# Kernel optimization log

Measured on AMD Instinct MI355X. Metric: run time of the kernel, lower is better.

Reference implementation:

```python
import jax, jax.numpy as jnp
import numpy as np

NEG = -9e15  # fill value used by the torch module for invalid band locations


def _sliding_window_attention(q, k, v, w, padding_mask):
    """Banded (Longformer-style) attention.
    q, k, v: [B, H, S, d]; padding_mask: [B, S] (nonzero = valid).
    S must be a multiple of 2*w (matches the no-extra-padding path of the
    original module). Returns context [B, H, S, d].
    """
    B, H, S, d = q.shape
    nb = S // w  # number of query blocks of size w
    # Query blocks: [B, H, nb, w, d]
    q_c = q.reshape(B, H, nb, w, d)
    # Each query block attends to a 3w-wide key/value slab (w halo each side).
    idx = (jnp.arange(nb) * w)[:, None] + jnp.arange(3 * w)[None, :]  # [nb, 3w]
    k_pad = jnp.pad(k, ((0, 0), (0, 0), (w, w), (0, 0)))
    v_pad = jnp.pad(v, ((0, 0), (0, 0), (w, w), (0, 0)))
    k_c = k_pad[:, :, idx, :]  # [B, H, nb, 3w, d]
    v_c = v_pad[:, :, idx, :]  # [B, H, nb, 3w, d]
    # Block scores: [B, H, nb, w, 3w]
    scores3 = jnp.einsum('bhnxd,bhnyd->bhnxy', q_c, k_c)
    # Extract the (2w+1)-wide band: query local x, band offset j -> slab col x+j
    x_idx = jnp.arange(w)[:, None]                     # [w, 1]
    j_idx = x_idx + jnp.arange(2 * w + 1)[None, :]     # [w, 2w+1], values in [0, 3w-1]
    band = scores3[..., x_idx, j_idx]                  # [B, H, nb, w, 2w+1]
    # Validity: global key position i - w + j must lie in [0, S) and be unpadded.
    key_pos = jnp.arange(S).reshape(nb, w)[:, :, None] - w + jnp.arange(2 * w + 1)
    valid = (key_pos >= 0) & (key_pos < S)                       # [nb, w, 2w+1]
    kmask = padding_mask[:, jnp.clip(key_pos, 0, S - 1)] != 0    # [B, nb, w, 2w+1]
    m = valid[None, None] & kmask[:, None]                       # [B, H, nb, w, 2w+1]
    band = jnp.where(m, band, NEG)
    # Original scales by sqrt(q.shape[-1]) == sqrt(head_dim)
    attn = jax.nn.softmax(band / jnp.sqrt(jnp.asarray(d, band.dtype)), axis=-1)
    attn = jnp.where(m, attn, 0.0)  # mirrors the explicit softmax_mask zeroing
    # Scatter band back to slab layout and contract with values.
    attn3 = jnp.zeros_like(scores3).at[..., x_idx, j_idx].set(attn)
    ctx = jnp.einsum('bhnxy,bhnyd->bhnxd', attn3, v_c)
    return ctx.reshape(B, H, S, d)


def setup_inputs() -> dict:
    key = jax.random.key(0)
    k0, k1, k2 = jax.random.split(key, 3)
    B, S, D, E = 2, 4096, 1024, 1024
    x = jax.random.normal(k0, (B, S, D), jnp.float32)
    padding_mask = jnp.ones((B, S), jnp.int32)
    # xavier_uniform like the torch _reset_parameters; biases zero
    s_qkv = (6.0 / (D + 3 * E)) ** 0.5
    Wqkv = jax.random.uniform(k1, (3 * E, D), jnp.float32, -s_qkv, s_qkv)
    bqkv = jnp.zeros((3 * E,), jnp.float32)
    s_o = (6.0 / (E + E)) ** 0.5
    Wo = jax.random.uniform(k2, (E, E), jnp.float32, -s_o, s_o)
    bo = jnp.zeros((E,), jnp.float32)
    return {'x': x, 'padding_mask': padding_mask, 'Wqkv': Wqkv, 'bqkv': bqkv,
            'Wo': Wo, 'bo': bo}


def reference(x, padding_mask, Wqkv, bqkv, Wo, bo):
    B, S, D = x.shape
    E = Wo.shape[0]
    H = 16
    hd = E // H
    w = 512 // 2  # window_size // 2
    qkv = (x @ Wqkv.T + bqkv).reshape(B, S, H, 3, hd)
    q = jnp.transpose(qkv[..., 0, :], (0, 2, 1, 3))  # [B, H, S, hd]
    k = jnp.transpose(qkv[..., 1, :], (0, 2, 1, 3))
    v = jnp.transpose(qkv[..., 2, :], (0, 2, 1, 3))
    ctx = _sliding_window_attention(q, k, v, w, padding_mask)
    out = jnp.transpose(ctx, (0, 2, 1, 3)).reshape(B, S, E)
    return out @ Wo.T + bo
```

## Files before the change

### kernel.cpp

```cpp
#include <hip/hip_runtime.h>
#include <stdint.h>

typedef __attribute__((ext_vector_type(8))) short short8;
typedef __attribute__((ext_vector_type(4))) float f32x4;

__device__ __forceinline__ unsigned short f2bf(float f) {
  unsigned int u = __builtin_bit_cast(unsigned int, f);
  u += 0x7FFFu + ((u >> 16) & 1u);
  return (unsigned short)(u >> 16);
}

#define GLD_LDS16(gp, lp) \
  __builtin_amdgcn_global_load_lds((const __attribute__((address_space(1))) void*)(gp), \
                                   (__attribute__((address_space(3))) void*)(lp), 16, 0, 0)

__global__ __launch_bounds__(256) void cvt_all_kernel(
    const float* __restrict__ x, const float* __restrict__ Wqkv, const float* __restrict__ Wo,
    unsigned short* __restrict__ xb, unsigned short* __restrict__ Wqkvb,
    unsigned short* __restrict__ Wob) {
  int i = blockIdx.x * 256 + threadIdx.x;
  const float* src; unsigned short* dst; int local; float scale = 1.0f;
  if (i < 1048576) { src = x; dst = xb; local = i; }
  else if (i < 1048576 + 393216) {
    local = i - 1048576; src = Wqkv; dst = Wqkvb;
    int row = (local * 8) >> 10;
    if (((row >> 6) % 3) == 0) scale = 0.125f;
  } else { local = i - 1441792; src = Wo; dst = Wob; }
  const float4* s4 = (const float4*)src;
  float4 a = s4[local * 2], b = s4[local * 2 + 1];
  uint4 o;
  o.x = (unsigned)f2bf(a.x * scale) | ((unsigned)f2bf(a.y * scale) << 16);
  o.y = (unsigned)f2bf(a.z * scale) | ((unsigned)f2bf(a.w * scale) << 16);
  o.z = (unsigned)f2bf(b.x * scale) | ((unsigned)f2bf(b.y * scale) << 16);
  o.w = (unsigned)f2bf(b.z * scale) | ((unsigned)f2bf(b.w * scale) << 16);
  *(uint4*)(dst + (size_t)local * 8) = o;
}

template<int EPI>
__global__ __launch_bounds__(256, 2) void gemm_bt(
    const unsigned short* __restrict__ A, const unsigned short* __restrict__ Bw,
    const float* __restrict__ bias, void* o0, void* o1, void* o2,
    int M, int N, int K, int nbc)
{
  __shared__ __align__(16) unsigned short Asm[128 * 64];
  __shared__ __align__(16) unsigned short Bsm[128 * 64];
  int bid = blockIdx.x;
  int bc = bid % nbc, br = bid / nbc;
  int tid = threadIdx.x;
  int lane = tid & 63, w = tid >> 6;
  int l16 = lane & 15, g = lane >> 4;
  int wr = w >> 1, wc = w & 1;
  f32x4 acc[4][4];
  #pragma unroll
  for (int i = 0; i < 4; i++)
    #pragma unroll
    for (int j = 0; j < 4; j++) acc[i][j] = (f32x4){0.f, 0.f, 0.f, 0.f};

  const int nkt = K >> 6;
  for (int kt = 0; kt < nkt; ++kt) {
    __syncthreads();
    #pragma unroll
    for (int r = 0; r < 4; ++r) {
      int idx = tid + 256 * r;
      int row = idx >> 3, s = idx & 7;
      int gofs = ((s ^ (row & 7)) << 3) + (kt << 6);
      GLD_LDS16(A + (size_t)(br * 128 + row) * K + gofs, &Asm[idx << 3]);
      GLD_LDS16(Bw + (size_t)(bc * 128 + row) * K + gofs, &Bsm[idx << 3]);
    }
    __syncthreads();
    #pragma unroll
    for (int kk = 0; kk < 2; ++kk) {
      short8 af[4], bf[4];
      #pragma unroll
      for (int i = 0; i < 4; i++) {
        int rowa = wr * 64 + i * 16 + l16;
        af[i] = *(const short8*)&Asm[(rowa << 6) + ((((kk << 2) + g) ^ (rowa & 7)) << 3)];
        int rowb = wc * 64 + i * 16 + l16;
        bf[i] = *(const short8*)&Bsm[(rowb << 6) + ((((kk << 2) + g) ^ (rowb & 7)) << 3)];
      }
      #pragma unroll
      for (int i = 0; i < 4; i++)
        #pragma unroll
        for (int j = 0; j < 4; j++)
          acc[i][j] = __builtin_amdgcn_mfma_f32_16x16x32_bf16(af[i], bf[j], acc[i][j], 0, 0, 0);
    }
  }
  #pragma unroll
  for (int i = 0; i < 4; i++) {
    #pragma unroll
    for (int j = 0; j < 4; j++) {
      int n = bc * 128 + wc * 64 + j * 16 + l16;
      int m0 = br * 128 + wr * 64 + i * 16 + g * 4;
      if (EPI == 0) {
        int t = (n >> 6) % 3;
        int hh = n / 192, e = n & 63;
        float bval = bias[n]; if (t == 0) bval *= 0.125f;
        int bb = m0 >> 12, s0 = m0 & 4095;
        if (t == 2) {
          unsigned short p0 = f2bf(acc[i][j][0] + bval);
          unsigned short p1 = f2bf(acc[i][j][1] + bval);
          unsigned short p2 = f2bf(acc[i][j][2] + bval);
          unsigned short p3 = f2bf(acc[i][j][3] + bval);
          uint2 pk;
          pk.x = (unsigned)p0 | ((unsigned)p1 << 16);
          pk.y = (unsigned)p2 | ((unsigned)p3 << 16);
          unsigned short* vt = (unsigned short*)o2;
          *(uint2*)&vt[(((size_t)(bb * 16 + hh) * 64 + e) << 12) + s0] = pk;
        } else {
          unsigned short* dst = (unsigned short*)(t == 0 ? o0 : o1);
          #pragma unroll
          for (int jj = 0; jj < 4; jj++)
            dst[((((size_t)(bb * 16 + hh) << 12) + s0 + jj) << 6) + e] = f2bf(acc[i][j][jj] + bval);
        }
      } else {
        float* o = (float*)o0;
        float bval = bias[n];
        #pragma unroll
        for (int jj = 0; jj < 4; jj++)
          o[(size_t)(m0 + jj) * N + n] = acc[i][j][jj] + bval;
      }
    }
  }
}

__global__ __launch_bounds__(256, 4) void attn_kernel(
    const unsigned short* __restrict__ qb, const unsigned short* __restrict__ kb,
    const unsigned short* __restrict__ vtb, const int* __restrict__ pmask,
    unsigned short* __restrict__ ctxb)
{
  const int S = 4096, HD = 64, WIN = 256;
  const float NEG = -1e38f;
  __shared__ __align__(16) unsigned short Ks[2][64 * 64];
  __shared__ __align__(16) unsigned short Vts[2][64 * 64];
  __shared__ __align__(16) unsigned short Ps[4][16 * 64];

  int bid0 = blockIdx.x;
  int bid = (bid0 & 7) * (gridDim.x >> 3) + (bid0 >> 3);
  int qt = bid & 63;
  int bh = bid >> 6;
  int b = bh >> 4, h = bh & 15;

  const unsigned short* Q  = qb + (size_t)bh * S * HD;
  const unsigned short* Kg = kb + (size_t)bh * S * HD;
  const unsigned short* Vt = vtb + (size_t)bh * HD * S;
  const int* pmrow = pmask + (size_t)b * S;

  int tid = threadIdx.x;
  int lane = tid & 63, w = tid >> 6;
  int l16 = lane & 15, g = lane >> 4;

  int q0 = qt * 64;
  int qw = q0 + w * 16;

  short8 qf[2];
  #pragma unroll
  for (int hh = 0; hh < 2; ++hh)
    qf[hh] = *(const short8*)&Q[(size_t)(qw + l16) * HD + hh * 32 + g * 8];

  f32x4 ctx[4];
  #pragma unroll
  for (int dt = 0; dt < 4; ++dt) ctx[dt] = (f32x4){0.f, 0.f, 0.f, 0.f};
  float lrun[4] = {0.f, 0.f, 0.f, 0.f};

  int kt0 = (q0 - WIN) >> 6; if (kt0 < 0) kt0 = 0;
  int kt1 = (q0 + 63 + WIN) >> 6; if (kt1 > 63) kt1 = 63;
  int nt = kt1 - kt0 + 1;

#define STAGE(BUF, KT) do {                                                       \
    int kb_ = (KT) * 64;                                                          \
    _Pragma("unroll")                                                             \
    for (int r_ = 0; r_ < 2; ++r_) {                                              \
      int idx_ = tid + 256 * r_;                                                  \
      int row_ = idx_ >> 3, s_ = idx_ & 7;                                        \
      int c_ = (s_ ^ (row_ & 7)) << 3;                                            \
      GLD_LDS16(Kg + (size_t)(kb_ + row_) * HD + c_, &Ks[BUF][idx_ << 3]);        \
      GLD_LDS16(Vt + (size_t)row_ * S + kb_ + c_, &Vts[BUF][idx_ << 3]);          \
    }                                                                             \
  } while (0)

  STAGE(0, kt0);
  asm volatile("s_waitcnt vmcnt(0)" ::: "memory");
  __syncthreads();

  int cur = 0;
  for (int it = 0; it < nt; ++it) {
    int kbase = (kt0 + it) * 64;
    if (it + 1 < nt) STAGE(cur ^ 1, kt0 + it + 1);

    float kbv[4];
    #pragma unroll
    for (int k4 = 0; k4 < 4; ++k4)
      kbv[k4] = (pmrow[kbase + k4 * 16 + l16] != 0) ? 0.f : NEG;

    f32x4 sc[4];
    __builtin_amdgcn_s_setprio(1);
    #pragma unroll
    for (int k4 = 0; k4 < 4; ++k4) {
      int krow = k4 * 16 + l16;
      f32x4 s = (f32x4){0.f, 0.f, 0.f, 0.f};
      short8 kf0 = *(const short8*)&Ks[cur][(krow << 6) + ((g ^ (l16 & 7)) << 3)];
      s = __builtin_amdgcn_mfma_f32_16x16x32_bf16(qf[0], kf0, s, 0, 0, 0);
      short8 kf1 = *(const short8*)&Ks[cur][(krow << 6) + (((4 + g) ^ (l16 & 7)) << 3)];
      s = __builtin_amdgcn_mfma_f32_16x16x32_bf16(qf[1], kf1, s, 0, 0, 0);
      sc[k4] = s;
    }
    __builtin_amdgcn_s_setprio(0);

    #pragma unroll
    for (int k4 = 0; k4 < 4; ++k4) {
      int kg = kbase + k4 * 16 + l16;
      #pragma unroll
      for (int jj = 0; jj < 4; ++jj) {
        int dq = kg - (qw + g * 4 + jj) + WIN;
        float sv = sc[k4][jj] + kbv[k4];
        sv = ((unsigned)dq <= 2u * WIN) ? sv : NEG;
        float p = __expf(sv);
        lrun[jj] += p;
        int row = g * 4 + jj, col = k4 * 16 + l16;
        Ps[w][(row << 6) + ((((col >> 3) ^ (row & 7)) << 3) | (col & 7))] = f2bf(p);
      }
    }

    asm volatile("s_waitcnt lgkmcnt(0)" ::: "memory");
    __builtin_amdgcn_sched_barrier(0);
    short8 pf0 = *(const short8*)&Ps[w][(l16 << 6) + ((g ^ (l16 & 7)) << 3)];
    short8 pf1 = *(const short8*)&Ps[w][(l16 << 6) + (((4 + g) ^ (l16 & 7)) << 3)];
    __builtin_amdgcn_s_setprio(1);
    #pragma unroll
    for (int dt = 0; dt < 4; ++dt) {
      int drow = dt * 16 + l16;
      short8 vf0 = *(const short8*)&Vts[cur][(drow << 6) + ((g ^ (drow & 7)) << 3)];
      ctx[dt] = __builtin_amdgcn_mfma_f32_16x16x32_bf16(pf0, vf0, ctx[dt], 0, 0, 0);
      short8 vf1 = *(const short8*)&Vts[cur][(drow << 6) + (((4 + g) ^ (drow & 7)) << 3)];
      ctx[dt] = __builtin_amdgcn_mfma_f32_16x16x32_bf16(pf1, vf1, ctx[dt], 0, 0, 0);
    }
    __builtin_amdgcn_s_setprio(0);

    if (it + 1 < nt) {
      asm volatile("s_waitcnt vmcnt(0)" ::: "memory");
      __syncthreads();
      cur ^= 1;
    }
  }
#undef STAGE

  #pragma unroll
  for (int jj = 0; jj < 4; ++jj) {
    float ps = lrun[jj];
    #pragma unroll
    for (int mk = 1; mk < 16; mk <<= 1) ps += __shfl_xor(ps, mk);
    lrun[jj] = ps;
  }

  #pragma unroll
  for (int jj = 0; jj < 4; ++jj) {
    float rc = (lrun[jj] > 0.f) ? (1.f / lrun[jj]) : 0.f;
    int qrow = qw + g * 4 + jj;
    size_t base = ((size_t)b * S + qrow) * 1024 + h * 64;
    #pragma unroll
    for (int dt = 0; dt < 4; ++dt)
      ctxb[base + dt * 16 + l16] = f2bf(ctx[dt][jj] * rc);
  }
}

extern "C" void kernel_launch(void* const* d_in, const int* in_sizes, int n_in,
                              void* d_out, int out_size, void* d_ws, size_t ws_size,
                              hipStream_t stream) {
  const float* x     = (const float*)d_in[0];
  const int*   pmask = (const int*)d_in[1];
  const float* Wqkv  = (const float*)d_in[2];
  const float* bqkv  = (const float*)d_in[3];
  const float* Wo    = (const float*)d_in[4];
  const float* bo    = (const float*)d_in[5];

  char* wsp = (char*)d_ws;
  unsigned short* xb    = (unsigned short*)(wsp);
  unsigned short* Wqkvb = (unsigned short*)(wsp + (size_t)(16u << 20));
  unsigned short* Wob   = (unsigned short*)(wsp + (size_t)(22u << 20));
  unsigned short* vtb   = (unsigned short*)(wsp + (size_t)(24u << 20));
  unsigned short* ctxb  = (unsigned short*)(wsp + (size_t)(40u << 20));
  unsigned short* qbuf  = (unsigned short*)d_out;
  unsigned short* kbuf  = (unsigned short*)d_out + (size_t)8388608;

  cvt_all_kernel<<<6144, 256, 0, stream>>>(x, Wqkv, Wo, xb, Wqkvb, Wob);

  gemm_bt<0><<<(8192 / 128) * (3072 / 128), 256, 0, stream>>>(
      xb, Wqkvb, bqkv, qbuf, kbuf, vtb, 8192, 3072, 1024, 3072 / 128);

  attn_kernel<<<2048, 256, 0, stream>>>(qbuf, kbuf, vtb, pmask, ctxb);

  gemm_bt<1><<<(8192 / 128) * (1024 / 128), 256, 0, stream>>>(
      ctxb, Wob, bo, d_out, nullptr, nullptr, 8192, 1024, 1024, 1024 / 128);
}
```

Before: 146.7 us.

## Enlarge attention query tile to 256 rows with 8 waves sharing K/V tiles

Each attention block now covers 256 queries with 512 threads (8 waves, 32 query rows each as two 16-row subtiles) instead of 64 queries with 4 waves. K/V tiles are staged once per block and reused across more queries, so the halo of redundant key/value loads per block shrinks from 9 tiles per 64 queries to 12 tiles per 256 queries. The cost is larger blocks, more registers per wave (double accumulators), a grid of only 512 blocks, and the 256-query tile overlapping more fully-masked key tiles at the band edges, which can waste MFMA work.

```diff
diff --git a/kernel.cpp b/kernel.cpp
--- a/kernel.cpp
+++ b/kernel.cpp
@@ -123,7 +123,7 @@
   }
 }
 
-__global__ __launch_bounds__(256, 4) void attn_kernel(
+__global__ __launch_bounds__(512, 6) void attn_kernel(
     const unsigned short* __restrict__ qb, const unsigned short* __restrict__ kb,
     const unsigned short* __restrict__ vtb, const int* __restrict__ pmask,
     unsigned short* __restrict__ ctxb)
@@ -132,12 +132,12 @@
   const float NEG = -1e38f;
   __shared__ __align__(16) unsigned short Ks[2][64 * 64];
   __shared__ __align__(16) unsigned short Vts[2][64 * 64];
-  __shared__ __align__(16) unsigned short Ps[4][16 * 64];
+  __shared__ __align__(16) unsigned short Ps[8][16 * 64];
 
   int bid0 = blockIdx.x;
   int bid = (bid0 & 7) * (gridDim.x >> 3) + (bid0 >> 3);
-  int qt = bid & 63;
-  int bh = bid >> 6;
+  int qt = bid & 15;
+  int bh = bid >> 4;
   int b = bh >> 4, h = bh & 15;
 
   const unsigned short* Q  = qb + (size_t)bh * S * HD;
@@ -149,33 +149,33 @@
   int lane = tid & 63, w = tid >> 6;
   int l16 = lane & 15, g = lane >> 4;
 
-  int q0 = qt * 64;
-  int qw = q0 + w * 16;
-
-  short8 qf[2];
-  #pragma unroll
-  for (int hh = 0; hh < 2; ++hh)
-    qf[hh] = *(const short8*)&Q[(size_t)(qw + l16) * HD + hh * 32 + g * 8];
-
-  f32x4 ctx[4];
-  #pragma unroll
-  for (int dt = 0; dt < 4; ++dt) ctx[dt] = (f32x4){0.f, 0.f, 0.f, 0.f};
-  float lrun[4] = {0.f, 0.f, 0.f, 0.f};
+  int q0 = qt * 256;
+  int qw = q0 + w * 32;
+
+  short8 qf[2][2];
+  #pragma unroll
+  for (int qs = 0; qs < 2; ++qs)
+    #pragma unroll
+    for (int hh = 0; hh < 2; ++hh)
+      qf[qs][hh] = *(const short8*)&Q[(size_t)(qw + qs * 16 + l16) * HD + hh * 32 + g * 8];
+
+  f32x4 ctx[2][4];
+  #pragma unroll
+  for (int qs = 0; qs < 2; ++qs)
+    #pragma unroll
+    for (int dt = 0; dt < 4; ++dt) ctx[qs][dt] = (f32x4){0.f, 0.f, 0.f, 0.f};
+  float lrun[2][4] = {{0.f,0.f,0.f,0.f},{0.f,0.f,0.f,0.f}};
 
   int kt0 = (q0 - WIN) >> 6; if (kt0 < 0) kt0 = 0;
-  int kt1 = (q0 + 63 + WIN) >> 6; if (kt1 > 63) kt1 = 63;
+  int kt1 = (q0 + 255 + WIN) >> 6; if (kt1 > 63) kt1 = 63;
   int nt = kt1 - kt0 + 1;
 
 #define STAGE(BUF, KT) do {                                                       \
     int kb_ = (KT) * 64;                                                          \
-    _Pragma("unroll")                                                             \
-    for (int r_ = 0; r_ < 2; ++r_) {                                              \
-      int idx_ = tid + 256 * r_;                                                  \
-      int row_ = idx_ >> 3, s_ = idx_ & 7;                                        \
-      int c_ = (s_ ^ (row_ & 7)) << 3;                                            \
-      GLD_LDS16(Kg + (size_t)(kb_ + row_) * HD + c_, &Ks[BUF][idx_ << 3]);        \
-      GLD_LDS16(Vt + (size_t)row_ * S + kb_ + c_, &Vts[BUF][idx_ << 3]);          \
-    }                                                                             \
+    int row_ = tid >> 3, s_ = tid & 7;                                            \
+    int c_ = (s_ ^ (row_ & 7)) << 3;                                              \
+    GLD_LDS16(Kg + (size_t)(kb_ + row_) * HD + c_, &Ks[BUF][tid << 3]);           \
+    GLD_LDS16(Vt + (size_t)row_ * S + kb_ + c_, &Vts[BUF][tid << 3]);             \
   } while (0)
 
   STAGE(0, kt0);
@@ -192,49 +192,53 @@
     for (int k4 = 0; k4 < 4; ++k4)
       kbv[k4] = (pmrow[kbase + k4 * 16 + l16] != 0) ? 0.f : NEG;
 
-    f32x4 sc[4];
-    __builtin_amdgcn_s_setprio(1);
-    #pragma unroll
-    for (int k4 = 0; k4 < 4; ++k4) {
-      int krow = k4 * 16 + l16;
-      f32x4 s = (f32x4){0.f, 0.f, 0.f, 0.f};
-      short8 kf0 = *(const short8*)&Ks[cur][(krow << 6) + ((g ^ (l16 & 7)) << 3)];
-      s = __builtin_amdgcn_mfma_f32_16x16x32_bf16(qf[0], kf0, s, 0, 0, 0);
-      short8 kf1 = *(const short8*)&Ks[cur][(krow << 6) + (((4 + g) ^ (l16 & 7)) << 3)];
-      s = __builtin_amdgcn_mfma_f32_16x16x32_bf16(qf[1], kf1, s, 0, 0, 0);
-      sc[k4] = s;
-    }
-    __builtin_amdgcn_s_setprio(0);
-
-    #pragma unroll
-    for (int k4 = 0; k4 < 4; ++k4) {
-      int kg = kbase + k4 * 16 + l16;
-      #pragma unroll
-      for (int jj = 0; jj < 4; ++jj) {
-        int dq = kg - (qw + g * 4 + jj) + WIN;
-        float sv = sc[k4][jj] + kbv[k4];
-        sv = ((unsigned)dq <= 2u * WIN) ? sv : NEG;
-        float p = __expf(sv);
-        lrun[jj] += p;
-        int row = g * 4 + jj, col = k4 * 16 + l16;
-        Ps[w][(row << 6) + ((((col >> 3) ^ (row & 7)) << 3) | (col & 7))] = f2bf(p);
-      }
-    }
-
-    asm volatile("s_waitcnt lgkmcnt(0)" ::: "memory");
-    __builtin_amdgcn_sched_barrier(0);
-    short8 pf0 = *(const short8*)&Ps[w][(l16 << 6) + ((g ^ (l16 & 7)) << 3)];
-    short8 pf1 = *(const short8*)&Ps[w][(l16 << 6) + (((4 + g) ^ (l16 & 7)) << 3)];
-    __builtin_amdgcn_s_setprio(1);
-    #pragma unroll
-    for (int dt = 0; dt < 4; ++dt) {
-      int drow = dt * 16 + l16;
-      short8 vf0 = *(const short8*)&Vts[cur][(drow << 6) + ((g ^ (drow & 7)) << 3)];
-      ctx[dt] = __builtin_amdgcn_mfma_f32_16x16x32_bf16(pf0, vf0, ctx[dt], 0, 0, 0);
-      short8 vf1 = *(const short8*)&Vts[cur][(drow << 6) + (((4 + g) ^ (drow & 7)) << 3)];
-      ctx[dt] = __builtin_amdgcn_mfma_f32_16x16x32_bf16(pf1, vf1, ctx[dt], 0, 0, 0);
-    }
-    __builtin_amdgcn_s_setprio(0);
+    #pragma unroll
+    for (int qs = 0; qs < 2; ++qs) {
+      f32x4 sc[4];
+      __builtin_amdgcn_s_setprio(1);
+      #pragma unroll
+      for (int k4 = 0; k4 < 4; ++k4) {
+        int krow = k4 * 16 + l16;
+        f32x4 s = (f32x4){0.f, 0.f, 0.f, 0.f};
+        short8 kf0 = *(const short8*)&Ks[cur][(krow << 6) + ((g ^ (l16 & 7)) << 3)];
+        s = __builtin_amdgcn_mfma_f32_16x16x32_bf16(qf[qs][0], kf0, s, 0, 0, 0);
+        short8 kf1 = *(const short8*)&Ks[cur][(krow << 6) + (((4 + g) ^ (l16 & 7)) << 3)];
+        s = __builtin_amdgcn_mfma_f32_16x16x32_bf16(qf[qs][1], kf1, s, 0, 0, 0);
+        sc[k4] = s;
+      }
+      __builtin_amdgcn_s_setprio(0);
+
+      int qbase = qw + qs * 16 + g * 4;
+      #pragma unroll
+      for (int k4 = 0; k4 < 4; ++k4) {
+        int kg = kbase + k4 * 16 + l16;
+        #pragma unroll
+        for (int jj = 0; jj < 4; ++jj) {
+          int dq = kg - (qbase + jj) + WIN;
+          float sv = sc[k4][jj] + kbv[k4];
+          sv = ((unsigned)dq <= 2u * WIN) ? sv : NEG;
+          float p = __expf(sv);
+          lrun[qs][jj] += p;
+          int row = g * 4 + jj, col = k4 * 16 + l16;
+          Ps[w][(row << 6) + ((((col >> 3) ^ (row & 7)) << 3) | (col & 7))] = f2bf(p);
+        }
+      }
+
+      asm volatile("s_waitcnt lgkmcnt(0)" ::: "memory");
+      __builtin_amdgcn_sched_barrier(0);
+      short8 pf0 = *(const short8*)&Ps[w][(l16 << 6) + ((g ^ (l16 & 7)) << 3)];
+      short8 pf1 = *(const short8*)&Ps[w][(l16 << 6) + (((4 + g) ^ (l16 & 7)) << 3)];
+      __builtin_amdgcn_s_setprio(1);
+      #pragma unroll
+      for (int dt = 0; dt < 4; ++dt) {
+        int drow = dt * 16 + l16;
+        short8 vf0 = *(const short8*)&Vts[cur][(drow << 6) + ((g ^ (drow & 7)) << 3)];
+        ctx[qs][dt] = __builtin_amdgcn_mfma_f32_16x16x32_bf16(pf0, vf0, ctx[qs][dt], 0, 0, 0);
+        short8 vf1 = *(const short8*)&Vts[cur][(drow << 6) + (((4 + g) ^ (drow & 7)) << 3)];
+        ctx[qs][dt] = __builtin_amdgcn_mfma_f32_16x16x32_bf16(pf1, vf1, ctx[qs][dt], 0, 0, 0);
+      }
+      __builtin_amdgcn_s_setprio(0);
+    }
 
     if (it + 1 < nt) {
       asm volatile("s_waitcnt vmcnt(0)" ::: "memory");
@@ -245,21 +249,19 @@
 #undef STAGE
 
   #pragma unroll
-  for (int jj = 0; jj < 4; ++jj) {
-    float ps = lrun[jj];
-    #pragma unroll
-    for (int mk = 1; mk < 16; mk <<= 1) ps += __shfl_xor(ps, mk);
-    lrun[jj] = ps;
-  }
-
-  #pragma unroll
-  for (int jj = 0; jj < 4; ++jj) {
-    float rc = (lrun[jj] > 0.f) ? (1.f / lrun[jj]) : 0.f;
-    int qrow = qw + g * 4 + jj;
-    size_t base = ((size_t)b * S + qrow) * 1024 + h * 64;
-    #pragma unroll
-    for (int dt = 0; dt < 4; ++dt)
-      ctxb[base + dt * 16 + l16] = f2bf(ctx[dt][jj] * rc);
+  for (int qs = 0; qs < 2; ++qs) {
+    #pragma unroll
+    for (int jj = 0; jj < 4; ++jj) {
+      float ps = lrun[qs][jj];
+      #pragma unroll
+      for (int mk = 1; mk < 16; mk <<= 1) ps += __shfl_xor(ps, mk);
+      float rc = (ps > 0.f) ? (1.f / ps) : 0.f;
+      int qrow = qw + qs * 16 + g * 4 + jj;
+      size_t base = ((size_t)b * S + qrow) * 1024 + h * 64;
+      #pragma unroll
+      for (int dt = 0; dt < 4; ++dt)
+        ctxb[base + dt * 16 + l16] = f2bf(ctx[qs][dt][jj] * rc);
+    }
   }
 }
 
@@ -287,7 +289,7 @@
   gemm_bt<0><<<(8192 / 128) * (3072 / 128), 256, 0, stream>>>(
       xb, Wqkvb, bqkv, qbuf, kbuf, vtb, 8192, 3072, 1024, 3072 / 128);
 
-  attn_kernel<<<2048, 256, 0, stream>>>(qbuf, kbuf, vtb, pmask, ctxb);
+  attn_kernel<<<512, 512, 0, stream>>>(qbuf, kbuf, vtb, pmask, ctxb);
 
   gemm_bt<1><<<(8192 / 128) * (1024 / 128), 256, 0, stream>>>(
       ctxb, Wob, bo, d_out, nullptr, nullptr, 8192, 1024, 1024, 1024 / 128);
```

Result: slower. 305.0 us (+108.0%).
